# Kernel tuning notes

Hardware: AMD Instinct MI355X
Metric: run time of the kernel (lower is better)

The kernel has to match this reference:

```python
import jax, jax.numpy as jnp
import numpy as np

B, H, W, C = 4, 64, 64, 256
D = C // 8  # reduction_ratio = 8


def setup_inputs() -> dict:
    key = jax.random.key(0)
    ks = jax.random.split(key, 6)
    scale = 1.0 / np.sqrt(C)
    return {
        "x": jax.random.normal(ks[0], (B, H, W, C), dtype=jnp.float32),
        "Wf": jax.random.normal(ks[1], (C, D), dtype=jnp.float32) * scale,
        "Wg": jax.random.normal(ks[2], (C, D), dtype=jnp.float32) * scale,
        "Wh": jax.random.normal(ks[3], (C, D), dtype=jnp.float32) * scale,
        "Wv": jax.random.normal(ks[4], (D, C), dtype=jnp.float32) * (1.0 / np.sqrt(D)),
        "gamma": jax.random.normal(ks[5], (), dtype=jnp.float32),
    }


def reference(x, Wf, Wg, Wh, Wv, gamma):
    b, h, w, c = x.shape
    n = h * w
    xf = x.reshape(b, n, c)
    # 1x1 convs (no bias) == per-pixel matmuls over channels
    q = xf @ Wf  # [b, n, d]
    k = xf @ Wg  # [b, n, d]
    v = xf @ Wh  # [b, n, d]
    # beta[i, j] = k_i . q_j ; softmax over last (query) axis, unscaled
    beta = jax.nn.softmax(jnp.einsum('bnd,bmd->bnm', k, q), axis=-1)  # [b, n, n]
    o = jnp.einsum('bnm,bmd->bnd', beta, v)  # [b, n, d]
    o = o.reshape(b, h, w, -1) @ Wv  # output 1x1 conv -> [b, h, w, c]
    return gamma * o + x
```

## Files before the change

kernel.cpp:

```cpp
#include <hip/hip_runtime.h>
#include <hip/hip_bf16.h>
#include <stdint.h>


typedef __attribute__((ext_vector_type(8))) short bf16x8;
typedef __attribute__((ext_vector_type(4))) float f32x4;
typedef unsigned short ushort_t;

static __device__ __forceinline__ ushort_t f2bf(float f) {
    __hip_bfloat16 h = __float2bfloat16(f);
    return __builtin_bit_cast(ushort_t, h);
}
static __device__ __forceinline__ float bf2f(ushort_t u) {
    return __bfloat162float(__builtin_bit_cast(__hip_bfloat16, u));
}

#define NROWS 16384
#define NTOK  4096
#define QKS   40
#define PVS   72
#define OPART (NROWS * 32)

__global__ __launch_bounds__(256) void qkv_kernel(
    const float* __restrict__ x,
    const float* __restrict__ Wf, const float* __restrict__ Wg,
    const float* __restrict__ Wh,
    ushort_t* __restrict__ qh,
    ushort_t* __restrict__ kh, ushort_t* __restrict__ kl,
    ushort_t* __restrict__ vT)
{
    __shared__ __align__(16) ushort_t xh[32 * QKS];
    __shared__ __align__(16) ushort_t xl[32 * QKS];

    const int tid  = threadIdx.x;
    const int wave = tid >> 6;
    const int lane = tid & 63;
    const int ln15 = lane & 15;
    const int quad = lane >> 4;
    const int row0 = blockIdx.x * 32;
    const int rg     = wave & 1;
    const int cgbase = wave >> 1;
    const int r  = tid >> 3;
    const int pp = (tid & 7) * 4;

    f32x4 acc[3];
    #pragma unroll
    for (int ci = 0; ci < 3; ++ci) acc[ci] = (f32x4){0.f, 0.f, 0.f, 0.f};

    float4 xa = *reinterpret_cast<const float4*>(&x[(row0 + r) * 256 + pp]);

    for (int k0 = 0; k0 < 256; k0 += 32) {
        bf16x8 bh[3], bl[3];
        #pragma unroll
        for (int ci = 0; ci < 3; ++ci) {
            int cg = cgbase + ci * 2;
            const float* Wsrc = (cg < 2) ? Wf : (cg < 4) ? Wg : Wh;
            int c = (cg & 1) * 16 + ln15;
            ushort_t hv8[8], lv8[8];
            #pragma unroll
            for (int j = 0; j < 8; ++j) {
                float w = Wsrc[(k0 + quad * 8 + j) * 32 + c];
                ushort_t hi = f2bf(w);
                hv8[j] = hi;
                lv8[j] = f2bf(w - bf2f(hi));
            }
            bh[ci] = *reinterpret_cast<bf16x8*>(hv8);
            bl[ci] = *reinterpret_cast<bf16x8*>(lv8);
        }
        float fv[4];
        *reinterpret_cast<float4*>(fv) = xa;
        ushort_t hv[4], lv[4];
        #pragma unroll
        for (int j = 0; j < 4; ++j) {
            hv[j] = f2bf(fv[j]);
            lv[j] = f2bf(fv[j] - bf2f(hv[j]));
        }
        __syncthreads();
        *reinterpret_cast<uint2*>(&xh[r * QKS + pp]) = *reinterpret_cast<uint2*>(hv);
        *reinterpret_cast<uint2*>(&xl[r * QKS + pp]) = *reinterpret_cast<uint2*>(lv);
        __syncthreads();
        if (k0 < 224)
            xa = *reinterpret_cast<const float4*>(&x[(row0 + r) * 256 + k0 + 32 + pp]);

        const bf16x8 ah = *reinterpret_cast<const bf16x8*>(
            &xh[(rg * 16 + ln15) * QKS + quad * 8]);
        const bf16x8 al = *reinterpret_cast<const bf16x8*>(
            &xl[(rg * 16 + ln15) * QKS + quad * 8]);
        #pragma unroll
        for (int ci = 0; ci < 3; ++ci) {
            acc[ci] = __builtin_amdgcn_mfma_f32_16x16x32_bf16(ah, bh[ci], acc[ci], 0, 0, 0);
            acc[ci] = __builtin_amdgcn_mfma_f32_16x16x32_bf16(al, bh[ci], acc[ci], 0, 0, 0);
            acc[ci] = __builtin_amdgcn_mfma_f32_16x16x32_bf16(ah, bl[ci], acc[ci], 0, 0, 0);
        }
    }

    #pragma unroll
    for (int ci = 0; ci < 3; ++ci) {
        int cg = cgbase + ci * 2;
        int cc = (cg & 1) * 16 + ln15;
        int rowb = row0 + rg * 16 + quad * 4;
        if (cg < 2) {
            #pragma unroll
            for (int rr = 0; rr < 4; ++rr)
                qh[(rowb + rr) * 32 + cc] = f2bf(acc[ci][rr]);
        } else if (cg < 4) {
            #pragma unroll
            for (int rr = 0; rr < 4; ++rr) {
                float val = acc[ci][rr];
                ushort_t hi = f2bf(val);
                kh[(rowb + rr) * 32 + cc] = hi;
                kl[(rowb + rr) * 32 + cc] = f2bf(val - bf2f(hi));
            }
        } else {
            int bb = row0 >> 12;
            int m  = (row0 & 4095) + rg * 16 + quad * 4;
            ushort4 h4;
            h4.x = f2bf(acc[ci][0]);
            h4.y = f2bf(acc[ci][1]);
            h4.z = f2bf(acc[ci][2]);
            h4.w = f2bf(acc[ci][3]);
            *reinterpret_cast<ushort4*>(&vT[bb * 131072 + cc * 4096 + m]) = h4;
        }
    }
}

__global__ __launch_bounds__(256, 4) void attn_kernel(
    const ushort_t* __restrict__ qhg,
    const ushort_t* __restrict__ khg, const ushort_t* __restrict__ klg,
    const ushort_t* __restrict__ vT,
    float* __restrict__ o_part, float* __restrict__ l_part)
{
    __shared__ __align__(16) ushort_t Khs[64 * QKS];
    __shared__ __align__(16) ushort_t Kls[64 * QKS];
    __shared__ __align__(16) ushort_t Qhs[2][64 * QKS];
    __shared__ __align__(16) ushort_t Vth[2][32 * PVS];
    __shared__ __align__(16) ushort_t Ps[4 * 16 * PVS];

    const int tid  = threadIdx.x;
    const int wave = tid >> 6;
    const int lane = tid & 63;
    const int ln15 = lane & 15;
    const int quad = lane >> 4;

    const int rowtile = blockIdx.x & 255;
    const int chunk   = blockIdx.x >> 8;
    const int b    = rowtile >> 6;
    const int n0   = (rowtile & 63) * 64;
    const int base = b * NTOK;
    const int bb   = b * 131072;
    const int mt0  = chunk * 16;

    const int r  = tid >> 2;
    const int p  = (tid & 3) * 8;
    const int vd = tid >> 3;
    const int vm = (tid & 7) * 8;

    {
        uint4 a0 = *reinterpret_cast<const uint4*>(&khg[(base + n0 + r) * 32 + p]);
        *reinterpret_cast<uint4*>(&Khs[r * QKS + p]) = a0;
        uint4 a1 = *reinterpret_cast<const uint4*>(&klg[(base + n0 + r) * 32 + p]);
        *reinterpret_cast<uint4*>(&Kls[r * QKS + p]) = a1;
    }
    {
        int m0 = mt0 * 64;
        uint4 t0 = *reinterpret_cast<const uint4*>(&qhg[(base + m0 + r) * 32 + p]);
        *reinterpret_cast<uint4*>(&Qhs[0][r * QKS + p]) = t0;
        uint4 v0 = *reinterpret_cast<const uint4*>(&vT[bb + vd * 4096 + m0 + vm]);
        *reinterpret_cast<uint4*>(&Vth[0][vd * PVS + vm]) = v0;
    }
    __syncthreads();

    const bf16x8 khf = *reinterpret_cast<const bf16x8*>(
        &Khs[(wave * 16 + ln15) * QKS + quad * 8]);
    const bf16x8 klf = *reinterpret_cast<const bf16x8*>(
        &Kls[(wave * 16 + ln15) * QKS + quad * 8]);

    f32x4 accO[2];
    accO[0] = (f32x4){0.f, 0.f, 0.f, 0.f};
    accO[1] = (f32x4){0.f, 0.f, 0.f, 0.f};
    float lacc[4] = {0.f, 0.f, 0.f, 0.f};

    int buf = 0;
    for (int it = 0; it < 16; ++it) {
        uint4 nqh, nvh;
        if (it < 15) {
            int m1 = (mt0 + it + 1) * 64;
            nqh = *reinterpret_cast<const uint4*>(&qhg[(base + m1 + r) * 32 + p]);
            nvh = *reinterpret_cast<const uint4*>(&vT[bb + vd * 4096 + m1 + vm]);
        }

        f32x4 st[4];
        #pragma unroll
        for (int t = 0; t < 4; ++t) {
            const bf16x8 qf = *reinterpret_cast<const bf16x8*>(
                &Qhs[buf][(t * 16 + ln15) * QKS + quad * 8]);
            f32x4 s = __builtin_amdgcn_mfma_f32_16x16x32_bf16(
                khf, qf, (f32x4){0.f, 0.f, 0.f, 0.f}, 0, 0, 0);
            s = __builtin_amdgcn_mfma_f32_16x16x32_bf16(klf, qf, s, 0, 0, 0);
            st[t] = s;
        }

        #pragma unroll
        for (int t = 0; t < 4; ++t)
            #pragma unroll
            for (int rr = 0; rr < 4; ++rr)
                st[t][rr] = __expf(st[t][rr]);
        #pragma unroll
        for (int rr = 0; rr < 4; ++rr)
            lacc[rr] += st[0][rr] + st[1][rr] + st[2][rr] + st[3][rr];

        ushort_t* pw = &Ps[wave * 16 * PVS];
        #pragma unroll
        for (int t = 0; t < 4; ++t)
            #pragma unroll
            for (int rr = 0; rr < 4; ++rr)
                pw[(quad * 4 + rr) * PVS + ((t ^ quad) & 3) * 16 + ln15] = f2bf(st[t][rr]);

        const int rq = (ln15 >> 2) & 3;
        #pragma unroll
        for (int kc = 0; kc < 2; ++kc) {
            const bf16x8 af = *reinterpret_cast<const bf16x8*>(
                &pw[ln15 * PVS + (((kc * 32 + quad * 8) ^ (rq * 16)))]);
            #pragma unroll
            for (int s01 = 0; s01 < 2; ++s01) {
                const bf16x8 bhf = *reinterpret_cast<const bf16x8*>(
                    &Vth[buf][(s01 * 16 + ln15) * PVS + kc * 32 + quad * 8]);
                accO[s01] = __builtin_amdgcn_mfma_f32_16x16x32_bf16(af, bhf, accO[s01], 0, 0, 0);
            }
        }

        if (it < 15) {
            *reinterpret_cast<uint4*>(&Qhs[buf ^ 1][r * QKS + p]) = nqh;
            *reinterpret_cast<uint4*>(&Vth[buf ^ 1][vd * PVS + vm]) = nvh;
            __syncthreads();
        }
        buf ^= 1;
    }

    #pragma unroll
    for (int rr = 0; rr < 4; ++rr) {
        float s0 = lacc[rr];
        #pragma unroll
        for (int off = 1; off < 16; off <<= 1)
            s0 += __shfl_xor(s0, off);
        lacc[rr] = s0;
    }
    const int row_base = base + n0 + wave * 16 + quad * 4;
    float* op = o_part + (size_t)chunk * OPART;
    if (ln15 == 0) {
        #pragma unroll
        for (int rr = 0; rr < 4; ++rr)
            l_part[chunk * NROWS + row_base + rr] = lacc[rr];
    }
    #pragma unroll
    for (int s01 = 0; s01 < 2; ++s01)
        #pragma unroll
        for (int rr = 0; rr < 4; ++rr)
            op[(row_base + rr) * 32 + s01 * 16 + ln15] = accO[s01][rr];
}

__global__ __launch_bounds__(256) void out_kernel(
    const float* __restrict__ o_part, const float* __restrict__ l_part,
    const float* __restrict__ Wv, const float* __restrict__ x,
    const float* __restrict__ gamma, float* __restrict__ out)
{
    __shared__ float wv[8192];
    __shared__ float orow[32][32];
    __shared__ float linv[32];
    const int tid  = threadIdx.x;
    const int row0 = blockIdx.x * 32;

    for (int i = tid; i < 8192; i += 256) wv[i] = Wv[i];
    for (int i = tid; i < 1024; i += 256) {
        int rr = i >> 5, d = i & 31;
        int idx = (row0 + rr) * 32 + d;
        orow[rr][d] = o_part[idx] + o_part[OPART + idx]
                    + o_part[2 * OPART + idx] + o_part[3 * OPART + idx];
    }
    if (tid < 32) {
        int row = row0 + tid;
        linv[tid] = 1.0f / (l_part[row] + l_part[NROWS + row]
                          + l_part[2 * NROWS + row] + l_part[3 * NROWS + row]);
    }
    __syncthreads();

    const float g = gamma[0];
    #pragma unroll 4
    for (int rc = 0; rc < 32; rc += 8) {
        float acc[8];
        #pragma unroll
        for (int rr = 0; rr < 8; ++rr) acc[rr] = 0.f;
        for (int d = 0; d < 32; ++d) {
            float wvd = wv[d * 256 + tid];
            #pragma unroll
            for (int rr = 0; rr < 8; ++rr) acc[rr] += orow[rc + rr][d] * wvd;
        }
        #pragma unroll
        for (int rr = 0; rr < 8; ++rr) {
            int row = row0 + rc + rr;
            out[row * 256 + tid] = g * acc[rr] * linv[rc + rr] + x[row * 256 + tid];
        }
    }
}

extern "C" void kernel_launch(void* const* d_in, const int* in_sizes, int n_in,
                              void* d_out, int out_size, void* d_ws, size_t ws_size,
                              hipStream_t stream)
{
    const float* x     = (const float*)d_in[0];
    const float* Wf    = (const float*)d_in[1];
    const float* Wg    = (const float*)d_in[2];
    const float* Wh    = (const float*)d_in[3];
    const float* Wv    = (const float*)d_in[4];
    const float* gamma = (const float*)d_in[5];
    float* out = (float*)d_out;

    ushort_t* qh = (ushort_t*)d_ws;
    ushort_t* kh = qh + NROWS * 32;
    ushort_t* kl = kh + NROWS * 32;
    ushort_t* vT = kl + NROWS * 32;
    float* o_part = (float*)(vT + NROWS * 32);
    float* l_part = o_part + (size_t)4 * OPART;

    qkv_kernel<<<dim3(512), dim3(256), 0, stream>>>(x, Wf, Wg, Wh, qh, kh, kl, vT);
    attn_kernel<<<dim3(1024), dim3(256), 0, stream>>>(qh, kh, kl, vT, o_part, l_part);
    out_kernel<<<dim3(512), dim3(256), 0, stream>>>(o_part, l_part, Wv, x, gamma, out);
}
```

Baseline: 124.4 us.

## Keep P in registers via transposed scores and split keys across waves

The attention kernel now computes the transposed scores (query x key) so the exp'd probabilities come out of the MFMA already in the B-operand layout of a 16x16x16 bf16 MFMA. P is fed straight from registers into the PV product, so the LDS round trip for P is gone. Each wave holds all 64 K rows in registers and handles its own 16-query slice per iteration, loading Q and V directly from global memory. This removes the per-iteration LDS staging, double buffering and __syncthreads. In exchange it needs a cross-wave LDS reduction of O and l at the end, more accumulator registers, and uncoalesced, non-prefetched global loads of V.

```diff
diff --git a/kernel.cpp b/kernel.cpp
--- a/kernel.cpp
+++ b/kernel.cpp
@@ -4,6 +4,7 @@
 
 
 typedef __attribute__((ext_vector_type(8))) short bf16x8;
+typedef __attribute__((ext_vector_type(4))) short bf16x4;
 typedef __attribute__((ext_vector_type(4))) float f32x4;
 typedef unsigned short ushort_t;
 
@@ -15,10 +16,20 @@
     return __bfloat162float(__builtin_bit_cast(__hip_bfloat16, u));
 }
 
+static __device__ __forceinline__ f32x4 mfma16bf(bf16x4 a, bf16x4 b, f32x4 c) {
+#if __has_builtin(__builtin_amdgcn_mfma_f32_16x16x16bf16_1k)
+    return __builtin_amdgcn_mfma_f32_16x16x16bf16_1k(a, b, c, 0, 0, 0);
+#else
+    f32x4 d;
+    asm("v_mfma_f32_16x16x16_bf16 %0, %1, %2, %3"
+        : "=v"(d) : "v"(a), "v"(b), "v"(c));
+    return d;
+#endif
+}
+
 #define NROWS 16384
 #define NTOK  4096
 #define QKS   40
-#define PVS   72
 #define OPART (NROWS * 32)
 
 __global__ __launch_bounds__(256) void qkv_kernel(
@@ -130,11 +141,8 @@
     const ushort_t* __restrict__ vT,
     float* __restrict__ o_part, float* __restrict__ l_part)
 {
-    __shared__ __align__(16) ushort_t Khs[64 * QKS];
-    __shared__ __align__(16) ushort_t Kls[64 * QKS];
-    __shared__ __align__(16) ushort_t Qhs[2][64 * QKS];
-    __shared__ __align__(16) ushort_t Vth[2][32 * PVS];
-    __shared__ __align__(16) ushort_t Ps[4 * 16 * PVS];
+    __shared__ float Ored[4][32][65];
+    __shared__ float Lred[4][64];
 
     const int tid  = threadIdx.x;
     const int wave = tid >> 6;
@@ -148,115 +156,92 @@
     const int n0   = (rowtile & 63) * 64;
     const int base = b * NTOK;
     const int bb   = b * 131072;
-    const int mt0  = chunk * 16;
-
-    const int r  = tid >> 2;
-    const int p  = (tid & 3) * 8;
-    const int vd = tid >> 3;
-    const int vm = (tid & 7) * 8;
-
-    {
-        uint4 a0 = *reinterpret_cast<const uint4*>(&khg[(base + n0 + r) * 32 + p]);
-        *reinterpret_cast<uint4*>(&Khs[r * QKS + p]) = a0;
-        uint4 a1 = *reinterpret_cast<const uint4*>(&klg[(base + n0 + r) * 32 + p]);
-        *reinterpret_cast<uint4*>(&Kls[r * QKS + p]) = a1;
-    }
-    {
-        int m0 = mt0 * 64;
-        uint4 t0 = *reinterpret_cast<const uint4*>(&qhg[(base + m0 + r) * 32 + p]);
-        *reinterpret_cast<uint4*>(&Qhs[0][r * QKS + p]) = t0;
-        uint4 v0 = *reinterpret_cast<const uint4*>(&vT[bb + vd * 4096 + m0 + vm]);
-        *reinterpret_cast<uint4*>(&Vth[0][vd * PVS + vm]) = v0;
+
+    bf16x8 khf[4], klf[4];
+    #pragma unroll
+    for (int t = 0; t < 4; ++t) {
+        khf[t] = *reinterpret_cast<const bf16x8*>(
+            &khg[(base + n0 + t * 16 + ln15) * 32 + quad * 8]);
+        klf[t] = *reinterpret_cast<const bf16x8*>(
+            &klg[(base + n0 + t * 16 + ln15) * 32 + quad * 8]);
+    }
+
+    f32x4 accO[2][4];
+    #pragma unroll
+    for (int s01 = 0; s01 < 2; ++s01)
+        #pragma unroll
+        for (int t = 0; t < 4; ++t)
+            accO[s01][t] = (f32x4){0.f, 0.f, 0.f, 0.f};
+    float lacc[4] = {0.f, 0.f, 0.f, 0.f};
+
+    const int mbase = chunk * 1024 + wave * 16;
+    const ushort_t* qp  = qhg + (size_t)(base + mbase + ln15) * 32 + quad * 8;
+    const ushort_t* vp0 = vT + bb + ln15 * 4096 + mbase + quad * 4;
+    const ushort_t* vp1 = vp0 + 16 * 4096;
+
+    for (int it = 0; it < 16; ++it) {
+        const bf16x8 qf  = *reinterpret_cast<const bf16x8*>(qp);
+        const bf16x4 va0 = *reinterpret_cast<const bf16x4*>(vp0);
+        const bf16x4 va1 = *reinterpret_cast<const bf16x4*>(vp1);
+        qp  += 64 * 32;
+        vp0 += 64;
+        vp1 += 64;
+
+        #pragma unroll
+        for (int t = 0; t < 4; ++t) {
+            f32x4 s = __builtin_amdgcn_mfma_f32_16x16x32_bf16(
+                qf, khf[t], (f32x4){0.f, 0.f, 0.f, 0.f}, 0, 0, 0);
+            s = __builtin_amdgcn_mfma_f32_16x16x32_bf16(qf, klf[t], s, 0, 0, 0);
+
+            float p0 = __expf(s[0]);
+            float p1 = __expf(s[1]);
+            float p2 = __expf(s[2]);
+            float p3 = __expf(s[3]);
+            lacc[t] += (p0 + p1) + (p2 + p3);
+
+            ushort_t pu[4];
+            pu[0] = f2bf(p0);
+            pu[1] = f2bf(p1);
+            pu[2] = f2bf(p2);
+            pu[3] = f2bf(p3);
+            const bf16x4 pb = *reinterpret_cast<bf16x4*>(pu);
+
+            accO[0][t] = mfma16bf(va0, pb, accO[0][t]);
+            accO[1][t] = mfma16bf(va1, pb, accO[1][t]);
+        }
+    }
+
+    #pragma unroll
+    for (int s01 = 0; s01 < 2; ++s01)
+        #pragma unroll
+        for (int t = 0; t < 4; ++t)
+            #pragma unroll
+            for (int rr = 0; rr < 4; ++rr)
+                Ored[wave][s01 * 16 + quad * 4 + rr][t * 16 + ln15] = accO[s01][t][rr];
+
+    #pragma unroll
+    for (int t = 0; t < 4; ++t) {
+        float v = lacc[t];
+        v += __shfl_xor(v, 16);
+        v += __shfl_xor(v, 32);
+        if (quad == 0) Lred[wave][t * 16 + ln15] = v;
     }
     __syncthreads();
 
-    const bf16x8 khf = *reinterpret_cast<const bf16x8*>(
-        &Khs[(wave * 16 + ln15) * QKS + quad * 8]);
-    const bf16x8 klf = *reinterpret_cast<const bf16x8*>(
-        &Kls[(wave * 16 + ln15) * QKS + quad * 8]);
-
-    f32x4 accO[2];
-    accO[0] = (f32x4){0.f, 0.f, 0.f, 0.f};
-    accO[1] = (f32x4){0.f, 0.f, 0.f, 0.f};
-    float lacc[4] = {0.f, 0.f, 0.f, 0.f};
-
-    int buf = 0;
-    for (int it = 0; it < 16; ++it) {
-        uint4 nqh, nvh;
-        if (it < 15) {
-            int m1 = (mt0 + it + 1) * 64;
-            nqh = *reinterpret_cast<const uint4*>(&qhg[(base + m1 + r) * 32 + p]);
-            nvh = *reinterpret_cast<const uint4*>(&vT[bb + vd * 4096 + m1 + vm]);
-        }
-
-        f32x4 st[4];
-        #pragma unroll
-        for (int t = 0; t < 4; ++t) {
-            const bf16x8 qf = *reinterpret_cast<const bf16x8*>(
-                &Qhs[buf][(t * 16 + ln15) * QKS + quad * 8]);
-            f32x4 s = __builtin_amdgcn_mfma_f32_16x16x32_bf16(
-                khf, qf, (f32x4){0.f, 0.f, 0.f, 0.f}, 0, 0, 0);
-            s = __builtin_amdgcn_mfma_f32_16x16x32_bf16(klf, qf, s, 0, 0, 0);
-            st[t] = s;
-        }
-
-        #pragma unroll
-        for (int t = 0; t < 4; ++t)
-            #pragma unroll
-            for (int rr = 0; rr < 4; ++rr)
-                st[t][rr] = __expf(st[t][rr]);
-        #pragma unroll
-        for (int rr = 0; rr < 4; ++rr)
-            lacc[rr] += st[0][rr] + st[1][rr] + st[2][rr] + st[3][rr];
-
-        ushort_t* pw = &Ps[wave * 16 * PVS];
-        #pragma unroll
-        for (int t = 0; t < 4; ++t)
-            #pragma unroll
-            for (int rr = 0; rr < 4; ++rr)
-                pw[(quad * 4 + rr) * PVS + ((t ^ quad) & 3) * 16 + ln15] = f2bf(st[t][rr]);
-
-        const int rq = (ln15 >> 2) & 3;
-        #pragma unroll
-        for (int kc = 0; kc < 2; ++kc) {
-            const bf16x8 af = *reinterpret_cast<const bf16x8*>(
-                &pw[ln15 * PVS + (((kc * 32 + quad * 8) ^ (rq * 16)))]);
-            #pragma unroll
-            for (int s01 = 0; s01 < 2; ++s01) {
-                const bf16x8 bhf = *reinterpret_cast<const bf16x8*>(
-                    &Vth[buf][(s01 * 16 + ln15) * PVS + kc * 32 + quad * 8]);
-                accO[s01] = __builtin_amdgcn_mfma_f32_16x16x32_bf16(af, bhf, accO[s01], 0, 0, 0);
-            }
-        }
-
-        if (it < 15) {
-            *reinterpret_cast<uint4*>(&Qhs[buf ^ 1][r * QKS + p]) = nqh;
-            *reinterpret_cast<uint4*>(&Vth[buf ^ 1][vd * PVS + vm]) = nvh;
-            __syncthreads();
-        }
-        buf ^= 1;
-    }
-
-    #pragma unroll
-    for (int rr = 0; rr < 4; ++rr) {
-        float s0 = lacc[rr];
-        #pragma unroll
-        for (int off = 1; off < 16; off <<= 1)
-            s0 += __shfl_xor(s0, off);
-        lacc[rr] = s0;
-    }
-    const int row_base = base + n0 + wave * 16 + quad * 4;
+    const int rowb = base + n0;
     float* op = o_part + (size_t)chunk * OPART;
-    if (ln15 == 0) {
-        #pragma unroll
-        for (int rr = 0; rr < 4; ++rr)
-            l_part[chunk * NROWS + row_base + rr] = lacc[rr];
-    }
-    #pragma unroll
-    for (int s01 = 0; s01 < 2; ++s01)
-        #pragma unroll
-        for (int rr = 0; rr < 4; ++rr)
-            op[(row_base + rr) * 32 + s01 * 16 + ln15] = accO[s01][rr];
+    #pragma unroll
+    for (int e = 0; e < 8; ++e) {
+        int idx = e * 256 + tid;
+        int d = idx & 31;
+        int n = idx >> 5;
+        float v = Ored[0][d][n] + Ored[1][d][n] + Ored[2][d][n] + Ored[3][d][n];
+        op[(rowb + n) * 32 + d] = v;
+    }
+    if (tid < 64) {
+        l_part[chunk * NROWS + rowb + tid] =
+            Lred[0][tid] + Lred[1][tid] + Lred[2][tid] + Lred[3][tid];
+    }
 }
 
 __global__ __launch_bounds__(256) void out_kernel(
```

Measured after the change: 122.7 us. No clear change (-1.4%).
